# Kernel optimization log

Measured on AMD Instinct MI355X. Metric: run time of the kernel, lower is better.

## Reference

```python
import jax, jax.numpy as jnp
from jax import lax
import numpy as np


def conv2d(x, w, pad):
    # x: NCHW, w: OIHW
    return lax.conv_general_dilated(
        x, w, window_strides=(1, 1), padding=[(pad, pad), (pad, pad)],
        dimension_numbers=("NCHW", "OIHW", "NCHW"))


def _scan_dir(x, a, axis, reverse):
    """Directional IRNN scan: cur = relu(x_i + alpha * prev), prev0 = 0.
    a broadcasts as (1, C, 1) over the remaining (B, C, L) slice dims."""
    if reverse:
        x = jnp.flip(x, axis)
    xs = jnp.moveaxis(x, axis, 0)  # (L, B, C, other)

    def step(prev, xi):
        cur = jax.nn.relu(xi + a * prev)
        return cur, cur

    _, hs = lax.scan(step, jnp.zeros_like(xs[0]), xs)
    h = jnp.moveaxis(hs, 0, axis)
    if reverse:
        h = jnp.flip(h, axis)
    return h


def spatial_irnn(x, alpha):
    a = alpha.reshape(1, -1, 1)  # broadcasts over (B, C, W) or (B, C, H)
    h_td = _scan_dir(x, a, axis=2, reverse=False)  # top -> down
    h_dt = _scan_dir(x, a, axis=2, reverse=True)   # down -> top
    h_lr = _scan_dir(x, a, axis=3, reverse=False)  # left -> right
    h_rl = _scan_dir(x, a, axis=3, reverse=True)   # right -> left
    return h_td, h_lr, h_dt, h_rl


def setup_inputs() -> dict:
    key = jax.random.key(0)
    ks = jax.random.split(key, 10)
    B, C, H, W = 8, 32, 256, 256
    mid = C // 2
    s = 0.05
    return {
        "x": jax.random.normal(ks[0], (B, C, H, W), jnp.float32),
        "alpha1": jnp.full((C,), 0.2, jnp.float32),
        "alpha2": jnp.full((C,), 0.2, jnp.float32),
        "w_in": jax.random.normal(ks[1], (C, C, 3, 3), jnp.float32) * s,
        "w2": jax.random.normal(ks[2], (C, 4 * C, 3, 3), jnp.float32) * s,
        "w3": jax.random.normal(ks[3], (C, 4 * C, 3, 3), jnp.float32) * s,
        "att_w1": jax.random.normal(ks[4], (mid, C, 3, 3), jnp.float32) * s,
        "att_w2": jax.random.normal(ks[5], (mid, mid, 3, 3), jnp.float32) * s,
        "att_w3": jax.random.normal(ks[6], (4, mid, 1, 1), jnp.float32) * s,
        "att_b3": jnp.zeros((4,), jnp.float32),
        "w_out": jax.random.normal(ks[7], (1, C, 1, 1), jnp.float32) * s,
    }


def reference(x, alpha1, alpha2, w_in, w2, w3, att_w1, att_w2, att_w3, att_b3, w_out):
    # Attention gate: 4 per-direction weight maps in (0,1)
    a = jax.nn.relu(conv2d(x, att_w1, pad=1))
    a = jax.nn.relu(conv2d(a, att_w2, pad=1))
    weight = jax.nn.sigmoid(conv2d(a, att_w3, pad=0) + att_b3.reshape(1, -1, 1, 1))

    def gate(up, right, down, left):
        return jnp.concatenate([
            up * weight[:, 0:1], right * weight[:, 1:2],
            down * weight[:, 2:3], left * weight[:, 3:4]], axis=1)

    out = conv2d(x, w_in, pad=1)
    up, right, down, left = spatial_irnn(out, alpha1)
    out = conv2d(gate(up, right, down, left), w2, pad=1)
    up, right, down, left = spatial_irnn(out, alpha2)
    out = jax.nn.relu(conv2d(gate(up, right, down, left), w3, pad=1))
    mask = jax.nn.sigmoid(conv2d(out, w_out, pad=0))
    return mask
```

## Files before the change

kernel.cpp:

```cpp
#include <hip/hip_runtime.h>
#include <cstddef>

#define H_ 256
#define W_ 256
#define HW_ 65536

typedef unsigned int uint;
typedef unsigned short ushort;
typedef __attribute__((ext_vector_type(8))) short short8;
typedef __attribute__((ext_vector_type(16))) float floatx16;

__device__ __forceinline__ float bf2f(ushort u) {
    return __uint_as_float(((uint)u) << 16);
}
__device__ __forceinline__ ushort f2bf(float f) {
    uint u = __float_as_uint(f);
    uint r = (u + 0x7fffu + ((u >> 16) & 1u)) >> 16;
    return (ushort)r;
}
__device__ __forceinline__ float sigmoidf_(float x) {
    return 1.0f / (1.0f + expf(-x));
}

#define GLOAD_LDS16(gsrc, ldst)                                                   \
    __builtin_amdgcn_global_load_lds(                                             \
        (const __attribute__((address_space(1))) void*)(gsrc),                    \
        (__attribute__((address_space(3))) void*)(ldst), 16, 0, 0)

#define IN_SLOTS 1408
#define W_SLOTS 1152
#define BUF_SLOTS 2560

__device__ __forceinline__ void prep_one(const float* src, ushort* dst,
                                         int CO, int CI, int e) {
    int chunk = e / 9216;
    int r = e - chunk * 9216;
    int co = r / 288;
    int kk = r - co * 288;
    int khw = kk >> 5;
    int ci = kk & 31;
    int cig = chunk * 32 + ci;
    float v = 0.f;
    if (co < CO && cig < CI) v = src[(co * CI + cig) * 9 + khw];
    int s = kk >> 4;
    int lane = ((kk >> 3) & 1) * 32 + co;
    int j = kk & 7;
    dst[(((size_t)chunk * 18 + s) * 64 + lane) * 8 + j] = f2bf(v);
}

__global__ __launch_bounds__(256) void prep_weights(
    const float* __restrict__ w_in, const float* __restrict__ w2,
    const float* __restrict__ w3, const float* __restrict__ aw1,
    const float* __restrict__ aw2,
    ushort* __restrict__ w_inB, ushort* __restrict__ w2B,
    ushort* __restrict__ w3B, ushort* __restrict__ aw1B,
    ushort* __restrict__ aw2B, ushort* __restrict__ zp) {
    int idx = blockIdx.x * 256 + threadIdx.x;
    if (idx < 64) zp[idx] = 0;
    if (idx < 9216)        prep_one(w_in, w_inB, 32, 32, idx);
    else if (idx < 46080)  prep_one(w2, w2B, 32, 128, idx - 9216);
    else if (idx < 82944)  prep_one(w3, w3B, 32, 128, idx - 46080);
    else if (idx < 92160)  prep_one(aw1, aw1B, 16, 32, idx - 82944);
    else if (idx < 101376) prep_one(aw2, aw2B, 16, 16, idx - 92160);
}

__global__ __launch_bounds__(256) void transform_x(const float* __restrict__ x,
                                                   ushort* __restrict__ xh) {
    __shared__ float s[64][33];
    const int t = threadIdx.x;
    const int w0 = blockIdx.x * 64, h = blockIdx.y, b = blockIdx.z;
    {
        int ww = t & 63, c0 = (t >> 6) * 8;
#pragma unroll
        for (int j = 0; j < 8; j++) {
            int c = c0 + j;
            s[ww][c] = x[((size_t)(b * 32 + c)) * HW_ + h * W_ + w0 + ww];
        }
    }
    __syncthreads();
    {
        int p = t >> 2, cb = t & 3;
        ushort tmp[8];
#pragma unroll
        for (int j = 0; j < 8; j++) tmp[j] = f2bf(s[p][cb * 8 + j]);
        *(uint4*)(xh + (((size_t)b * HW_ + h * W_ + w0 + p) * 32) + cb * 8) =
            *(const uint4*)tmp;
    }
}

struct StageDescL {
    uint goff[6];
    uint goffT[6];
    bool ok[6];
};
__device__ __forceinline__ void make_descL(StageDescL& d, int t, int w0, int h0, int b) {
#pragma unroll
    for (int i = 0; i < 6; i++) {
        int u = (i < 5) ? (i * 256 + t) : (1280 + t);
        int row = u / 136;
        int rem = u - row * 136;
        int p = rem >> 2, q = rem & 3;
        int cb = q ^ (p & 3) ^ ((p >> 2) & 3);
        int gh = h0 - 1 + row, gw = w0 - 1 + p;
        d.ok[i] = (u < 1360) && ((unsigned)gh < 256u) && ((unsigned)gw < 256u);
        d.goff[i]  = d.ok[i] ? (((uint)b * HW_ + (uint)gh * W_ + (uint)gw) * 32 + cb * 8) : 0u;
        d.goffT[i] = d.ok[i] ? (((uint)b * HW_ + (uint)gw * W_ + (uint)gh) * 32 + cb * 8) : 0u;
    }
}
__device__ __forceinline__ void stage_input(ushort* ibuf, const StageDescL& d,
                                            const ushort* __restrict__ inp,
                                            const ushort* __restrict__ zp,
                                            int t, int wid, bool tr) {
#pragma unroll
    for (int i = 0; i < 5; i++) {
        const ushort* src = d.ok[i] ? (inp + (tr ? d.goffT[i] : d.goff[i])) : zp;
        GLOAD_LDS16(src, ibuf + (size_t)(i * 256 + t) * 8);
    }
    if (wid < 2) {
        const ushort* src = d.ok[5] ? (inp + (tr ? d.goffT[5] : d.goff[5])) : zp;
        GLOAD_LDS16(src, ibuf + (size_t)(1280 + t) * 8);
    }
}
__device__ __forceinline__ void stage_wts(ushort* wbuf,
                                          const ushort* __restrict__ wsrc,
                                          int t, int wid) {
#pragma unroll
    for (int j = 0; j < 4; j++)
        GLOAD_LDS16(wsrc + (size_t)(j * 256 + t) * 8,
                    wbuf + (size_t)(j * 256 + t) * 8);
    if (wid >= 2)
        GLOAD_LDS16(wsrc + (size_t)(1024 + t - 128) * 8,
                    wbuf + (size_t)(1024 + t - 128) * 8);
}

__device__ __forceinline__ void mfma_chunk(const ushort* ibuf, const ushort* wbuf,
                                           int lco, int lhalf, int wid, int lane,
                                           floatx16& acc0, floatx16& acc1) {
#pragma unroll
    for (int half = 0; half < 2; half++) {
        short8 bf[9];
#pragma unroll
        for (int j = 0; j < 9; j++)
            bf[j] = *(const short8*)(wbuf + (size_t)((2 * j + half) * 64 + lane) * 8);
        const int cbr = half * 2 + lhalf;
#pragma unroll
        for (int kw = 0; kw < 3; kw++) {
            const int ww = lco + kw;
            const int cbs = cbr ^ (ww & 3) ^ ((ww >> 2) & 3);
            short8 a[4];
#pragma unroll
            for (int r = 0; r < 4; r++)
                a[r] = *(const short8*)(ibuf + (size_t)((wid * 2 + r) * 136 + (ww << 2) + cbs) * 8);
#pragma unroll
            for (int kh = 0; kh < 3; kh++) {
                acc0 = __builtin_amdgcn_mfma_f32_32x32x16_bf16(a[kh], bf[kh * 3 + kw], acc0, 0, 0, 0);
                acc1 = __builtin_amdgcn_mfma_f32_32x32x16_bf16(a[kh + 1], bf[kh * 3 + kw], acc1, 0, 0, 0);
            }
        }
    }
}

template<int NCHUNK, int EPI, bool RELU>
__global__ __launch_bounds__(256, (NCHUNK > 1) ? 2 : 4) void conv_mfma(
    const ushort* __restrict__ in0, const ushort* __restrict__ in1,
    const ushort* __restrict__ in2, const ushort* __restrict__ in3,
    const ushort* __restrict__ wB, const ushort* __restrict__ zp,
    ushort* __restrict__ outp, const float* __restrict__ aux_w,
    const float* __restrict__ aux_b) {
    constexpr int NBUF = (NCHUNK > 1) ? 2 : 1;
    __shared__ __align__(16) ushort smem[NBUF][BUF_SLOTS * 8];
    const int t = threadIdx.x;
    const int wid = t >> 6;
    const int lane = t & 63;
    const int lco = lane & 31, lhalf = lane >> 5;
    const int w0 = blockIdx.x * 32, h0 = blockIdx.y * 8, b = blockIdx.z;
    const ushort* ins[4] = {in0, in1, in2, in3};

    StageDescL d;
    make_descL(d, t, w0, h0, b);

    floatx16 acc0, acc1;
#pragma unroll
    for (int i = 0; i < 16; i++) { acc0[i] = 0.f; acc1[i] = 0.f; }

    stage_input(smem[0], d, ins[0], zp, t, wid, false);
    stage_wts(smem[0] + IN_SLOTS * 8, wB, t, wid);

    if constexpr (NCHUNK == 1) {
        __syncthreads();
        mfma_chunk(smem[0], smem[0] + IN_SLOTS * 8, lco, lhalf, wid, lane, acc0, acc1);
    } else {
#pragma unroll
        for (int ch = 0; ch < NCHUNK; ch++) {
            asm volatile("s_waitcnt lgkmcnt(0)" ::: "memory");
            __builtin_amdgcn_s_barrier();
            if (ch + 1 < NCHUNK) {
                stage_input(smem[(ch + 1) & 1], d, ins[ch + 1], zp, t, wid,
                            ((ch + 1) & 1) != 0);
                stage_wts(smem[(ch + 1) & 1] + IN_SLOTS * 8,
                          wB + (size_t)(ch + 1) * 9216, t, wid);
                asm volatile("s_waitcnt vmcnt(10)" ::: "memory");
            } else {
                asm volatile("s_waitcnt vmcnt(0)" ::: "memory");
            }
            __builtin_amdgcn_s_barrier();
            mfma_chunk(smem[ch & 1], smem[ch & 1] + IN_SLOTS * 8,
                       lco, lhalf, wid, lane, acc0, acc1);
        }
    }

    if (EPI == 0) {
#pragma unroll
        for (int r = 0; r < 16; r++) {
            int wl = (r & 3) + 8 * (r >> 2) + 4 * lhalf;
            float v0 = acc0[r], v1 = acc1[r];
            if (RELU) { v0 = fmaxf(v0, 0.f); v1 = fmaxf(v1, 0.f); }
            size_t p0 = (((size_t)b * HW_ + (h0 + wid * 2) * W_ + w0 + wl) * 32) + lco;
            outp[p0] = f2bf(v0);
            outp[p0 + (size_t)W_ * 32] = f2bf(v1);
        }
    } else {
        __syncthreads();
        ushort* ep = &smem[0][0];
#pragma unroll
        for (int r = 0; r < 16; r++) {
            int wl = (r & 3) + 8 * (r >> 2) + 4 * lhalf;
            float v0 = acc0[r], v1 = acc1[r];
            if (RELU) { v0 = fmaxf(v0, 0.f); v1 = fmaxf(v1, 0.f); }
            int pix0 = (wid * 2) * 32 + wl;
            ep[(size_t)pix0 * 40 + lco] = f2bf(v0);
            ep[(size_t)(pix0 + 32) * 40 + lco] = f2bf(v1);
        }
        __syncthreads();
        const ushort* tp = ep + (size_t)t * 40;
        if (EPI == 1) {
            float xin[16];
            uint4 q0 = *(const uint4*)tp;
            uint4 q1 = *(const uint4*)(tp + 8);
            const ushort* u0 = (const ushort*)&q0;
            const ushort* u1 = (const ushort*)&q1;
#pragma unroll
            for (int j = 0; j < 8; j++) { xin[j] = bf2f(u0[j]); xin[8 + j] = bf2f(u1[j]); }
            size_t pix = (size_t)b * HW_ + (size_t)(h0 + (t >> 5)) * W_ + w0 + (t & 31);
#pragma unroll
            for (int g = 0; g < 4; g++) {
                float acc = aux_b[g];
#pragma unroll
                for (int ci = 0; ci < 16; ci++) acc = fmaf(xin[ci], aux_w[g * 16 + ci], acc);
                outp[(size_t)g * 8 * HW_ + pix] = f2bf(sigmoidf_(acc));
            }
        } else {
            float acc = 0.f;
#pragma unroll
            for (int q = 0; q < 4; q++) {
                uint4 qv = *(const uint4*)(tp + q * 8);
                const ushort* uq = (const ushort*)&qv;
#pragma unroll
                for (int j = 0; j < 8; j++) acc = fmaf(bf2f(uq[j]), aux_w[q * 8 + j], acc);
            }
            float* fo = (float*)outp;
            fo[(size_t)b * HW_ + (size_t)(h0 + (t >> 5)) * W_ + w0 + (t & 31)] = sigmoidf_(acc);
        }
    }
}

__global__ __launch_bounds__(256, 2) void conv_dual(
    const ushort* __restrict__ in0, const ushort* __restrict__ wBa,
    const ushort* __restrict__ wBb, const ushort* __restrict__ zp,
    ushort* __restrict__ outA, ushort* __restrict__ outB) {
    __shared__ __align__(16) ushort smem[(IN_SLOTS + 2 * W_SLOTS) * 8];
    const int t = threadIdx.x;
    const int wid = t >> 6;
    const int lane = t & 63;
    const int lco = lane & 31, lhalf = lane >> 5;
    const int w0 = blockIdx.x * 32, h0 = blockIdx.y * 8, b = blockIdx.z;

    StageDescL d;
    make_descL(d, t, w0, h0, b);

    floatx16 accA0, accA1, accB0, accB1;
#pragma unroll
    for (int i = 0; i < 16; i++) { accA0[i] = 0.f; accA1[i] = 0.f; accB0[i] = 0.f; accB1[i] = 0.f; }

    stage_input(smem, d, in0, zp, t, wid, false);
    stage_wts(smem + IN_SLOTS * 8, wBa, t, wid);
    stage_wts(smem + (IN_SLOTS + W_SLOTS) * 8, wBb, t, wid);
    __syncthreads();
    mfma_chunk(smem, smem + IN_SLOTS * 8, lco, lhalf, wid, lane, accA0, accA1);
    mfma_chunk(smem, smem + (IN_SLOTS + W_SLOTS) * 8, lco, lhalf, wid, lane, accB0, accB1);

#pragma unroll
    for (int r = 0; r < 16; r++) {
        int wl = (r & 3) + 8 * (r >> 2) + 4 * lhalf;
        size_t p0 = (((size_t)b * HW_ + (h0 + wid * 2) * W_ + w0 + wl) * 32) + lco;
        outA[p0] = f2bf(accA0[r]);
        outA[p0 + (size_t)W_ * 32] = f2bf(accA1[r]);
        outB[p0] = f2bf(fmaxf(accB0[r], 0.f));
        outB[p0 + (size_t)W_ * 32] = f2bf(fmaxf(accB1[r], 0.f));
    }
}

template<int VERT>
__device__ __forceinline__ void scan_body(
    const ushort* __restrict__ feat, const float* __restrict__ alpha,
    const ushort* __restrict__ wmapT, ushort* __restrict__ gfwd,
    ushort* __restrict__ gbwd, int gf, int gb, int dir, int seg,
    int cgp, int b, int t) {
    const int cg = t & 3;
    const int col = cgp * 64 + (t >> 2);
    const int c0 = cg * 8;

    float a[8];
#pragma unroll
    for (int j = 0; j < 8; j++) a[j] = alpha[c0 + j];

    const ushort* wplane = wmapT + (size_t)(dir ? gb : gf) * 8 * HW_ + (size_t)b * HW_;
    ushort* gout = dir ? gbwd : gfwd;

    const int main0 = seg * 32;
    const int start = (seg == 0) ? 0 : main0 - 8;
    const int cnt = main0 - start + 32;

    auto pixR = [&](int p) -> size_t {
        int phys = dir ? 255 - p : p;
        return VERT ? ((size_t)phys * W_ + col) : ((size_t)col * W_ + phys);
    };
    auto pixW = [&](int p) -> size_t {
        int phys = dir ? 255 - p : p;
        return (size_t)phys * W_ + col;
    };

    uint4 xv[4];
    ushort wv[4];
#pragma unroll
    for (int k = 0; k < 4; k++) {
        size_t pix = pixR(start + k);
        xv[k] = *(const uint4*)(feat + ((size_t)b * HW_ + pix) * 32 + c0);
        wv[k] = wplane[pix];
    }
    float prev[8];
#pragma unroll
    for (int j = 0; j < 8; j++) prev[j] = 0.f;

    for (int i = 0; i < cnt; i += 4) {
#pragma unroll
        for (int k = 0; k < 4; k++) {
            const int p = start + i + k;
            uint4 xcur = xv[k];
            ushort wcur = wv[k];
            if (i + k + 4 < cnt) {
                size_t pix = pixR(p + 4);
                xv[k] = *(const uint4*)(feat + ((size_t)b * HW_ + pix) * 32 + c0);
                wv[k] = wplane[pix];
            }
            const ushort* xu = (const ushort*)&xcur;
            if (p >= main0) {
                float wmv = bf2f(wcur);
                ushort o[8];
#pragma unroll
                for (int j = 0; j < 8; j++) {
                    float cur = fmaxf(fmaf(a[j], prev[j], bf2f(xu[j])), 0.f);
                    prev[j] = cur;
                    o[j] = f2bf(cur * wmv);
                }
                *(uint4*)(gout + ((size_t)b * HW_ + pixW(p)) * 32 + c0) = *(const uint4*)o;
            } else {
#pragma unroll
                for (int j = 0; j < 8; j++)
                    prev[j] = fmaxf(fmaf(a[j], prev[j], bf2f(xu[j])), 0.f);
            }
        }
    }
}

__global__ __launch_bounds__(256) void scan_both(
    const ushort* __restrict__ feat, const float* __restrict__ alpha,
    const ushort* __restrict__ wmapT, ushort* __restrict__ g0,
    ushort* __restrict__ g1, ushort* __restrict__ g2, ushort* __restrict__ g3) {
    const int bx = blockIdx.x & 255;
    const int cgp = bx & 3;
    const int seg = (bx >> 2) & 7;
    const int b = bx >> 5;
    const int t = threadIdx.x;
    if (blockIdx.x < 256) {
        scan_body<1>(feat, alpha, wmapT, g0, g2, 0, 2, 0, seg, cgp, b, t);
        scan_body<1>(feat, alpha, wmapT, g0, g2, 0, 2, 1, 7 - seg, cgp, b, t);
    } else {
        scan_body<0>(feat, alpha, wmapT, g1, g3, 1, 3, 0, seg, cgp, b, t);
        scan_body<0>(feat, alpha, wmapT, g1, g3, 1, 3, 1, 7 - seg, cgp, b, t);
    }
}

extern "C" void kernel_launch(void* const* d_in, const int* in_sizes, int n_in,
                              void* d_out, int out_size, void* d_ws, size_t ws_size,
                              hipStream_t stream) {
    const float* x      = (const float*)d_in[0];
    const float* alpha1 = (const float*)d_in[1];
    const float* alpha2 = (const float*)d_in[2];
    const float* w_in   = (const float*)d_in[3];
    const float* w2     = (const float*)d_in[4];
    const float* w3     = (const float*)d_in[5];
    const float* aw1    = (const float*)d_in[6];
    const float* aw2    = (const float*)d_in[7];
    const float* aw3    = (const float*)d_in[8];
    const float* ab3    = (const float*)d_in[9];
    const float* wout   = (const float*)d_in[10];
    float* out = (float*)d_out;

    const size_t TEN = (size_t)8 * HW_ * 32;
    ushort* p = (ushort*)d_ws;
    ushort* xh    = p; p += TEN;
    ushort* feat  = p; p += TEN;
    ushort* g0    = p; p += TEN;
    ushort* g1    = p; p += TEN;
    ushort* g2    = p; p += TEN;
    ushort* g3    = p; p += TEN;
    ushort* wmapT = p; p += (size_t)4 * 8 * HW_;
    ushort* w_inB = p; p += 9216;
    ushort* w2B   = p; p += 36864;
    ushort* w3B   = p; p += 36864;
    ushort* aw1B  = p; p += 9216;
    ushort* aw2B  = p; p += 9216;
    ushort* zp    = p; p += 64;
    ushort* a1z   = g1;

    prep_weights<<<396, 256, 0, stream>>>(w_in, w2, w3, aw1, aw2,
                                          w_inB, w2B, w3B, aw1B, aw2B, zp);
    transform_x<<<dim3(4, 256, 8), 256, 0, stream>>>(x, xh);

    dim3 gconv(8, 32, 8);

    conv_dual<<<gconv, 256, 0, stream>>>(xh, w_inB, aw1B, zp, feat, a1z);
    conv_mfma<1, 1, true><<<gconv, 256, 0, stream>>>(a1z, a1z, a1z, a1z, aw2B, zp,
                                                     wmapT, aw3, ab3);

    scan_both<<<512, 256, 0, stream>>>(feat, alpha1, wmapT, g0, g1, g2, g3);

    conv_mfma<4, 0, false><<<gconv, 256, 0, stream>>>(g0, g1, g2, g3, w2B, zp,
                                                      feat, nullptr, nullptr);

    scan_both<<<512, 256, 0, stream>>>(feat, alpha2, wmapT, g0, g1, g2, g3);

    conv_mfma<4, 2, true><<<gconv, 256, 0, stream>>>(g0, g1, g2, g3, w3B, zp,
                                                     (ushort*)out, wout, nullptr);
}
```

Measured before the change: 340.4 us.

## Enlarge conv tiles to 16 rows per block with four accumulators per wave

Each convolution block now covers 16 output rows instead of 8. Every wave computes 4 rows and reuses each staged weight fragment across 4 MFMAs and each input row fragment across more outputs, which cuts the halo overhead from 10/8 to 18/16. The input LDS buffer and the staging loop grow, and the vmcnt waits are retuned to match. The larger tile raises register and LDS use, so occupancy drops (launch bounds lowered), and the grid is halved to 1024 blocks.

```diff
diff --git a/kernel.cpp b/kernel.cpp
--- a/kernel.cpp
+++ b/kernel.cpp
@@ -27,9 +27,11 @@
         (const __attribute__((address_space(1))) void*)(gsrc),                    \
         (__attribute__((address_space(3))) void*)(ldst), 16, 0, 0)
 
-#define IN_SLOTS 1408
+#define IN_SLOTS 2560
+#define IN_VALID 2448
+#define NSTG_IN 10
 #define W_SLOTS 1152
-#define BUF_SLOTS 2560
+#define BUF_SLOTS 3712
 
 __device__ __forceinline__ void prep_one(const float* src, ushort* dst,
                                          int CO, int CI, int e) {
@@ -89,20 +91,20 @@
 }
 
 struct StageDescL {
-    uint goff[6];
-    uint goffT[6];
-    bool ok[6];
+    uint goff[NSTG_IN];
+    uint goffT[NSTG_IN];
+    bool ok[NSTG_IN];
 };
 __device__ __forceinline__ void make_descL(StageDescL& d, int t, int w0, int h0, int b) {
 #pragma unroll
-    for (int i = 0; i < 6; i++) {
-        int u = (i < 5) ? (i * 256 + t) : (1280 + t);
+    for (int i = 0; i < NSTG_IN; i++) {
+        int u = i * 256 + t;
         int row = u / 136;
         int rem = u - row * 136;
         int p = rem >> 2, q = rem & 3;
         int cb = q ^ (p & 3) ^ ((p >> 2) & 3);
         int gh = h0 - 1 + row, gw = w0 - 1 + p;
-        d.ok[i] = (u < 1360) && ((unsigned)gh < 256u) && ((unsigned)gw < 256u);
+        d.ok[i] = (u < IN_VALID) && ((unsigned)gh < 256u) && ((unsigned)gw < 256u);
         d.goff[i]  = d.ok[i] ? (((uint)b * HW_ + (uint)gh * W_ + (uint)gw) * 32 + cb * 8) : 0u;
         d.goffT[i] = d.ok[i] ? (((uint)b * HW_ + (uint)gw * W_ + (uint)gh) * 32 + cb * 8) : 0u;
     }
@@ -110,15 +112,11 @@
 __device__ __forceinline__ void stage_input(ushort* ibuf, const StageDescL& d,
                                             const ushort* __restrict__ inp,
                                             const ushort* __restrict__ zp,
-                                            int t, int wid, bool tr) {
-#pragma unroll
-    for (int i = 0; i < 5; i++) {
+                                            int t, bool tr) {
+#pragma unroll
+    for (int i = 0; i < NSTG_IN; i++) {
         const ushort* src = d.ok[i] ? (inp + (tr ? d.goffT[i] : d.goff[i])) : zp;
         GLOAD_LDS16(src, ibuf + (size_t)(i * 256 + t) * 8);
-    }
-    if (wid < 2) {
-        const ushort* src = d.ok[5] ? (inp + (tr ? d.goffT[5] : d.goff[5])) : zp;
-        GLOAD_LDS16(src, ibuf + (size_t)(1280 + t) * 8);
     }
 }
 __device__ __forceinline__ void stage_wts(ushort* wbuf,
@@ -133,9 +131,9 @@
                     wbuf + (size_t)(1024 + t - 128) * 8);
 }
 
-__device__ __forceinline__ void mfma_chunk(const ushort* ibuf, const ushort* wbuf,
-                                           int lco, int lhalf, int wid, int lane,
-                                           floatx16& acc0, floatx16& acc1) {
+__device__ __forceinline__ void mfma_chunk4(const ushort* ibuf, const ushort* wbuf,
+                                            int lco, int lhalf, int wid, int lane,
+                                            floatx16* acc) {
 #pragma unroll
     for (int half = 0; half < 2; half++) {
         short8 bf[9];
@@ -147,21 +145,23 @@
         for (int kw = 0; kw < 3; kw++) {
             const int ww = lco + kw;
             const int cbs = cbr ^ (ww & 3) ^ ((ww >> 2) & 3);
-            short8 a[4];
-#pragma unroll
-            for (int r = 0; r < 4; r++)
-                a[r] = *(const short8*)(ibuf + (size_t)((wid * 2 + r) * 136 + (ww << 2) + cbs) * 8);
+            short8 a[6];
+#pragma unroll
+            for (int r = 0; r < 6; r++)
+                a[r] = *(const short8*)(ibuf + (size_t)((wid * 4 + r) * 136 + (ww << 2) + cbs) * 8);
 #pragma unroll
             for (int kh = 0; kh < 3; kh++) {
-                acc0 = __builtin_amdgcn_mfma_f32_32x32x16_bf16(a[kh], bf[kh * 3 + kw], acc0, 0, 0, 0);
-                acc1 = __builtin_amdgcn_mfma_f32_32x32x16_bf16(a[kh + 1], bf[kh * 3 + kw], acc1, 0, 0, 0);
+#pragma unroll
+                for (int j = 0; j < 4; j++)
+                    acc[j] = __builtin_amdgcn_mfma_f32_32x32x16_bf16(
+                        a[kh + j], bf[kh * 3 + kw], acc[j], 0, 0, 0);
             }
         }
     }
 }
 
 template<int NCHUNK, int EPI, bool RELU>
-__global__ __launch_bounds__(256, (NCHUNK > 1) ? 2 : 4) void conv_mfma(
+__global__ __launch_bounds__(256, (NCHUNK > 1) ? 1 : 2) void conv_mfma(
     const ushort* __restrict__ in0, const ushort* __restrict__ in1,
     const ushort* __restrict__ in2, const ushort* __restrict__ in3,
     const ushort* __restrict__ wB, const ushort* __restrict__ zp,
@@ -173,93 +173,105 @@
     const int wid = t >> 6;
     const int lane = t & 63;
     const int lco = lane & 31, lhalf = lane >> 5;
-    const int w0 = blockIdx.x * 32, h0 = blockIdx.y * 8, b = blockIdx.z;
+    const int w0 = blockIdx.x * 32, h0 = blockIdx.y * 16, b = blockIdx.z;
     const ushort* ins[4] = {in0, in1, in2, in3};
 
     StageDescL d;
     make_descL(d, t, w0, h0, b);
 
-    floatx16 acc0, acc1;
-#pragma unroll
-    for (int i = 0; i < 16; i++) { acc0[i] = 0.f; acc1[i] = 0.f; }
-
-    stage_input(smem[0], d, ins[0], zp, t, wid, false);
+    floatx16 acc[4];
+#pragma unroll
+    for (int j = 0; j < 4; j++)
+#pragma unroll
+        for (int i = 0; i < 16; i++) acc[j][i] = 0.f;
+
+    stage_input(smem[0], d, ins[0], zp, t, false);
     stage_wts(smem[0] + IN_SLOTS * 8, wB, t, wid);
 
     if constexpr (NCHUNK == 1) {
         __syncthreads();
-        mfma_chunk(smem[0], smem[0] + IN_SLOTS * 8, lco, lhalf, wid, lane, acc0, acc1);
+        mfma_chunk4(smem[0], smem[0] + IN_SLOTS * 8, lco, lhalf, wid, lane, acc);
     } else {
 #pragma unroll
         for (int ch = 0; ch < NCHUNK; ch++) {
             asm volatile("s_waitcnt lgkmcnt(0)" ::: "memory");
             __builtin_amdgcn_s_barrier();
             if (ch + 1 < NCHUNK) {
-                stage_input(smem[(ch + 1) & 1], d, ins[ch + 1], zp, t, wid,
+                stage_input(smem[(ch + 1) & 1], d, ins[ch + 1], zp, t,
                             ((ch + 1) & 1) != 0);
                 stage_wts(smem[(ch + 1) & 1] + IN_SLOTS * 8,
                           wB + (size_t)(ch + 1) * 9216, t, wid);
-                asm volatile("s_waitcnt vmcnt(10)" ::: "memory");
+                if (wid < 2) asm volatile("s_waitcnt vmcnt(14)" ::: "memory");
+                else         asm volatile("s_waitcnt vmcnt(15)" ::: "memory");
             } else {
                 asm volatile("s_waitcnt vmcnt(0)" ::: "memory");
             }
             __builtin_amdgcn_s_barrier();
-            mfma_chunk(smem[ch & 1], smem[ch & 1] + IN_SLOTS * 8,
-                       lco, lhalf, wid, lane, acc0, acc1);
+            mfma_chunk4(smem[ch & 1], smem[ch & 1] + IN_SLOTS * 8,
+                        lco, lhalf, wid, lane, acc);
         }
     }
 
     if (EPI == 0) {
 #pragma unroll
-        for (int r = 0; r < 16; r++) {
-            int wl = (r & 3) + 8 * (r >> 2) + 4 * lhalf;
-            float v0 = acc0[r], v1 = acc1[r];
-            if (RELU) { v0 = fmaxf(v0, 0.f); v1 = fmaxf(v1, 0.f); }
-            size_t p0 = (((size_t)b * HW_ + (h0 + wid * 2) * W_ + w0 + wl) * 32) + lco;
-            outp[p0] = f2bf(v0);
-            outp[p0 + (size_t)W_ * 32] = f2bf(v1);
+        for (int j = 0; j < 4; j++) {
+#pragma unroll
+            for (int r = 0; r < 16; r++) {
+                int wl = (r & 3) + 8 * (r >> 2) + 4 * lhalf;
+                float v = acc[j][r];
+                if (RELU) v = fmaxf(v, 0.f);
+                size_t p0 = (((size_t)b * HW_ + (h0 + wid * 4 + j) * W_ + w0 + wl) * 32) + lco;
+                outp[p0] = f2bf(v);
+            }
         }
     } else {
         __syncthreads();
         ushort* ep = &smem[0][0];
 #pragma unroll
-        for (int r = 0; r < 16; r++) {
-            int wl = (r & 3) + 8 * (r >> 2) + 4 * lhalf;
-            float v0 = acc0[r], v1 = acc1[r];
-            if (RELU) { v0 = fmaxf(v0, 0.f); v1 = fmaxf(v1, 0.f); }
-            int pix0 = (wid * 2) * 32 + wl;
-            ep[(size_t)pix0 * 40 + lco] = f2bf(v0);
-            ep[(size_t)(pix0 + 32) * 40 + lco] = f2bf(v1);
+        for (int j = 0; j < 4; j++) {
+#pragma unroll
+            for (int r = 0; r < 16; r++) {
+                int wl = (r & 3) + 8 * (r >> 2) + 4 * lhalf;
+                float v = acc[j][r];
+                if (RELU) v = fmaxf(v, 0.f);
+                int pix0 = (wid * 4 + j) * 32 + wl;
+                ep[(size_t)pix0 * 40 + lco] = f2bf(v);
+            }
         }
         __syncthreads();
-        const ushort* tp = ep + (size_t)t * 40;
-        if (EPI == 1) {
-            float xin[16];
-            uint4 q0 = *(const uint4*)tp;
-            uint4 q1 = *(const uint4*)(tp + 8);
-            const ushort* u0 = (const ushort*)&q0;
-            const ushort* u1 = (const ushort*)&q1;
-#pragma unroll
-            for (int j = 0; j < 8; j++) { xin[j] = bf2f(u0[j]); xin[8 + j] = bf2f(u1[j]); }
-            size_t pix = (size_t)b * HW_ + (size_t)(h0 + (t >> 5)) * W_ + w0 + (t & 31);
-#pragma unroll
-            for (int g = 0; g < 4; g++) {
-                float acc = aux_b[g];
-#pragma unroll
-                for (int ci = 0; ci < 16; ci++) acc = fmaf(xin[ci], aux_w[g * 16 + ci], acc);
-                outp[(size_t)g * 8 * HW_ + pix] = f2bf(sigmoidf_(acc));
-            }
-        } else {
-            float acc = 0.f;
-#pragma unroll
-            for (int q = 0; q < 4; q++) {
-                uint4 qv = *(const uint4*)(tp + q * 8);
-                const ushort* uq = (const ushort*)&qv;
-#pragma unroll
-                for (int j = 0; j < 8; j++) acc = fmaf(bf2f(uq[j]), aux_w[q * 8 + j], acc);
-            }
-            float* fo = (float*)outp;
-            fo[(size_t)b * HW_ + (size_t)(h0 + (t >> 5)) * W_ + w0 + (t & 31)] = sigmoidf_(acc);
+#pragma unroll
+        for (int pp = 0; pp < 2; pp++) {
+            const int pix = pp * 256 + t;
+            const ushort* tp = ep + (size_t)pix * 40;
+            const int prow = pix >> 5, pcol = pix & 31;
+            if (EPI == 1) {
+                float xin[16];
+                uint4 q0 = *(const uint4*)tp;
+                uint4 q1 = *(const uint4*)(tp + 8);
+                const ushort* u0 = (const ushort*)&q0;
+                const ushort* u1 = (const ushort*)&q1;
+#pragma unroll
+                for (int j = 0; j < 8; j++) { xin[j] = bf2f(u0[j]); xin[8 + j] = bf2f(u1[j]); }
+                size_t pixg = (size_t)b * HW_ + (size_t)(h0 + prow) * W_ + w0 + pcol;
+#pragma unroll
+                for (int g = 0; g < 4; g++) {
+                    float a1 = aux_b[g];
+#pragma unroll
+                    for (int ci = 0; ci < 16; ci++) a1 = fmaf(xin[ci], aux_w[g * 16 + ci], a1);
+                    outp[(size_t)g * 8 * HW_ + pixg] = f2bf(sigmoidf_(a1));
+                }
+            } else {
+                float a1 = 0.f;
+#pragma unroll
+                for (int q = 0; q < 4; q++) {
+                    uint4 qv = *(const uint4*)(tp + q * 8);
+                    const ushort* uq = (const ushort*)&qv;
+#pragma unroll
+                    for (int j = 0; j < 8; j++) a1 = fmaf(bf2f(uq[j]), aux_w[q * 8 + j], a1);
+                }
+                float* fo = (float*)outp;
+                fo[(size_t)b * HW_ + (size_t)(h0 + prow) * W_ + w0 + pcol] = sigmoidf_(a1);
+            }
         }
     }
 }
@@ -273,30 +285,33 @@
     const int wid = t >> 6;
     const int lane = t & 63;
     const int lco = lane & 31, lhalf = lane >> 5;
-    const int w0 = blockIdx.x * 32, h0 = blockIdx.y * 8, b = blockIdx.z;
+    const int w0 = blockIdx.x * 32, h0 = blockIdx.y * 16, b = blockIdx.z;
 
     StageDescL d;
     make_descL(d, t, w0, h0, b);
 
-    floatx16 accA0, accA1, accB0, accB1;
-#pragma unroll
-    for (int i = 0; i < 16; i++) { accA0[i] = 0.f; accA1[i] = 0.f; accB0[i] = 0.f; accB1[i] = 0.f; }
-
-    stage_input(smem, d, in0, zp, t, wid, false);
+    floatx16 accA[4], accB[4];
+#pragma unroll
+    for (int j = 0; j < 4; j++)
+#pragma unroll
+        for (int i = 0; i < 16; i++) { accA[j][i] = 0.f; accB[j][i] = 0.f; }
+
+    stage_input(smem, d, in0, zp, t, false);
     stage_wts(smem + IN_SLOTS * 8, wBa, t, wid);
     stage_wts(smem + (IN_SLOTS + W_SLOTS) * 8, wBb, t, wid);
     __syncthreads();
-    mfma_chunk(smem, smem + IN_SLOTS * 8, lco, lhalf, wid, lane, accA0, accA1);
-    mfma_chunk(smem, smem + (IN_SLOTS + W_SLOTS) * 8, lco, lhalf, wid, lane, accB0, accB1);
-
-#pragma unroll
-    for (int r = 0; r < 16; r++) {
-        int wl = (r & 3) + 8 * (r >> 2) + 4 * lhalf;
-        size_t p0 = (((size_t)b * HW_ + (h0 + wid * 2) * W_ + w0 + wl) * 32) + lco;
-        outA[p0] = f2bf(accA0[r]);
-        outA[p0 + (size_t)W_ * 32] = f2bf(accA1[r]);
-        outB[p0] = f2bf(fmaxf(accB0[r], 0.f));
-        outB[p0 + (size_t)W_ * 32] = f2bf(fmaxf(accB1[r], 0.f));
+    mfma_chunk4(smem, smem + IN_SLOTS * 8, lco, lhalf, wid, lane, accA);
+    mfma_chunk4(smem, smem + (IN_SLOTS + W_SLOTS) * 8, lco, lhalf, wid, lane, accB);
+
+#pragma unroll
+    for (int j = 0; j < 4; j++) {
+#pragma unroll
+        for (int r = 0; r < 16; r++) {
+            int wl = (r & 3) + 8 * (r >> 2) + 4 * lhalf;
+            size_t p0 = (((size_t)b * HW_ + (h0 + wid * 4 + j) * W_ + w0 + wl) * 32) + lco;
+            outA[p0] = f2bf(accA[j][r]);
+            outB[p0] = f2bf(fmaxf(accB[j][r], 0.f));
+        }
     }
 }
 
@@ -428,7 +443,7 @@
                                           w_inB, w2B, w3B, aw1B, aw2B, zp);
     transform_x<<<dim3(4, 256, 8), 256, 0, stream>>>(x, xh);
 
-    dim3 gconv(8, 32, 8);
+    dim3 gconv(8, 16, 8);
 
     conv_dual<<<gconv, 256, 0, stream>>>(xh, w_inB, aw1B, zp, feat, a1z);
     conv_mfma<1, 1, true><<<gconv, 256, 0, stream>>>(a1z, a1z, a1z, a1z, aw2B, zp,
```

New measurement: 367.4 us. +7.9%, slower.
